# Kernel tuning notes

Measured on AMD Instinct MI355X. Metric: run time of the kernel, lower is better.

## Reference

```python
import jax, jax.numpy as jnp
import numpy as np
from jax import lax

EPS = 1e-5

# int4 fake-quant (Brevitas-style, per-tensor float scale)
# signed act: [-8, 7]; unsigned act: [0, 15]; weight narrow-range: [-7, 7]

def ste_round(x):
    # straight-through round (matches Brevitas STE; forward math == round)
    return x + lax.stop_gradient(jnp.round(x) - x)

def fq(x, s, lo, hi):
    return jnp.clip(ste_round(x / s), lo, hi) * s

def qw(w):
    # Int4WeightQuant: per-tensor scale from max-abs stats, narrow range [-7,7]
    s = jnp.max(jnp.abs(w)) / 7.0
    return jnp.clip(ste_round(w / s), -7.0, 7.0) * s

def conv(x, w, pad):
    return lax.conv_general_dilated(x, w, (1, 1), pad,
                                    dimension_numbers=('NCHW', 'OIHW', 'NCHW'))

def maxpool2(x):
    return lax.reduce_window(x, -jnp.inf, lax.max, (1, 1, 2, 2), (1, 1, 2, 2), 'VALID')

def bn_apply(x, bn):
    g, b, m, v = bn[0], bn[1], bn[2], bn[3]
    inv = g / jnp.sqrt(v + EPS)
    return x * inv[None, :, None, None] + (b - m * inv)[None, :, None, None]

def block(x, w, bn, s_in, s_relu, pool):
    x = fq(x, s_in, -8.0, 7.0)          # conv input_quant (signed int4)
    x = conv(x, qw(w), 'SAME')          # 3x3 quant conv, no bias
    x = bn_apply(x, bn)                 # BatchNorm (eval, running stats)
    x = jax.nn.relu(x)
    x = fq(x, s_relu, 0.0, 15.0)        # QuantReLU (unsigned int4)
    return maxpool2(x) if pool else x

def _forward(x, ws, b9, bns, scales):
    x = fq(x, scales[0], -8.0, 7.0)     # QuantIdentity (signed int4)
    for i in range(8):
        x = block(x, ws[i], bns[i], scales[1 + i], scales[10 + i], pool=(i < 4))
    x = fq(x, scales[9], -8.0, 7.0)     # head input_quant
    x = conv(x, qw(ws[8]), 'VALID') + b9[None, :, None, None]  # 1x1 head with bias
    return x


def setup_inputs() -> dict:
    key = jax.random.key(0)
    ks = jax.random.split(key, 32)
    B, H, W = 16, 320, 640
    x = jax.random.normal(ks[0], (B, 3, H, W), dtype=jnp.float32)
    wshapes = [(16, 3, 3, 3), (32, 16, 3, 3), (64, 32, 3, 3)] + [(64, 64, 3, 3)] * 5 + [(36, 64, 1, 1)]
    inp = {'x': x}
    for i, sh in enumerate(wshapes):
        inp[f'w{i+1}'] = 0.05 * jax.random.normal(ks[1 + i], sh, dtype=jnp.float32)
    inp['b9'] = 0.01 * jax.random.normal(ks[10], (36,), dtype=jnp.float32)
    chans = [16, 32, 64, 64, 64, 64, 64, 64]
    for i, c in enumerate(chans):
        k1, k2, k3, k4 = jax.random.split(ks[11 + i], 4)
        g = 0.75 + 0.5 * jax.random.uniform(k1, (c,), dtype=jnp.float32)
        b = 0.1 * jax.random.normal(k2, (c,), dtype=jnp.float32)
        m = 0.1 * jax.random.normal(k3, (c,), dtype=jnp.float32)
        v = 0.5 + 0.5 * jax.random.uniform(k4, (c,), dtype=jnp.float32)
        inp[f'bn{i+1}'] = jnp.stack([g, b, m, v])  # (4, C)
    inp['scales'] = 0.02 + 0.1 * jax.random.uniform(ks[30], (18,), dtype=jnp.float32)
    return inp


def reference(x, w1, w2, w3, w4, w5, w6, w7, w8, w9, b9,
              bn1, bn2, bn3, bn4, bn5, bn6, bn7, bn8, scales):
    ws = [w1, w2, w3, w4, w5, w6, w7, w8, w9]
    bns = [bn1, bn2, bn3, bn4, bn5, bn6, bn7, bn8]
    return _forward(x, ws, b9, bns, scales)
```

## Files before the change

### kernel.cpp

```cpp
#include <hip/hip_runtime.h>
#include <stdint.h>

#define EPSV 1e-5f

typedef int v4i __attribute__((ext_vector_type(4)));

__device__ __forceinline__ v4i mfma16(v4i a, v4i b, v4i c) {
    return __builtin_amdgcn_mfma_i32_16x16x64_i8(a, b, c, 0, 0, 0);
}

__device__ __forceinline__ int8_t q_epi(int s, float fscale, float inv, float beta,
                                        float s_relu, float s_next)
{
#pragma clang fp contract(off)
    float y = (float)s * fscale;
    y = y * inv;
    y = y + beta;
    float r = rintf(y / s_relu);
    r = fminf(fmaxf(r, 0.f), 15.f);
    float v = r * s_relu;
    float r2 = rintf(v / s_next);
    r2 = fminf(fmaxf(r2, -8.f), 7.f);
    return (int8_t)(int)r2;
}

struct WPtrs { const float* w[9]; int n[9]; };

__global__ __launch_bounds__(256) void k_wmax(WPtrs a, unsigned* __restrict__ smax)
{
    const int t = blockIdx.y;
    const int n = a.n[t];
    const float* w = a.w[t];
    float m = 0.f;
    for (int i = blockIdx.x * 256 + threadIdx.x; i < n; i += 16 * 256)
        m = fmaxf(m, fabsf(w[i]));
#pragma unroll
    for (int off = 32; off > 0; off >>= 1) m = fmaxf(m, __shfl_down(m, off));
    __shared__ float red[4];
    if ((threadIdx.x & 63) == 0) red[threadIdx.x >> 6] = m;
    __syncthreads();
    if (threadIdx.x == 0) {
        m = fmaxf(fmaxf(red[0], red[1]), fmaxf(red[2], red[3]));
        atomicMax(smax + t, __float_as_uint(m));
    }
}

struct PackArgs {
    const float* w[9];
    const float* bn[8];
    const unsigned* smax;
    int* qw;
    float* bnp;
};

#define NB_B    207
#define NB_HEAD 3
#define NB_BN   2

__global__ __launch_bounds__(256) void k_pack(PackArgs a)
{
#pragma clang fp contract(off)
    const int blk = blockIdx.x;
    if (blk < NB_B) {
        const int u = blk * 256 + threadIdx.x;
        const int bcum[9] = {0, 256, 1792, 6912, 16128, 25344, 34560, 43776, 52992};
        const int CIGA[8] = {1, 4, 8, 16, 16, 16, 16, 16};
        const int COA[8]  = {16, 32, 64, 64, 64, 64, 64, 64};
        const int NTA[8]  = {1, 2, 4, 4, 4, 4, 4, 4};
        const int CINA[8] = {3, 16, 32, 64, 64, 64, 64, 64};
        int L = 0;
        while (u >= bcum[L + 1]) ++L;
        const int rem = u - bcum[L];
        const int d = rem & 3;
        const int lane = (rem >> 2) & 63;
        const int gnt = rem >> 8;
        const int NT = NTA[L];
        const int nt = gnt % NT;
        const int g = gnt / NT;
        const int CIG = CIGA[L], CIN = CINA[L], CO = COA[L];
        const int TG = 16 / CIG;
        const int n = nt * 16 + (lane & 15);
        const float s = __uint_as_float(a.smax[L]) / 7.0f;
        const float* w = a.w[L];
        unsigned dw = 0;
        for (int jb = 0; jb < 4; ++jb) {
            const int k = 16 * (lane >> 4) + 4 * d + jb;
            const int tap = g * TG + k / (4 * CIG);
            const int ci = k % (4 * CIG);
            int qv = 0;
            if (tap < 9 && ci < CIN && n < CO) {
                float rr = rintf(w[(n * CIN + ci) * 9 + tap] / s);
                rr = fminf(fmaxf(rr, -7.f), 7.f);
                qv = (int)rr;
            }
            dw |= ((unsigned)(qv & 0xff)) << (8 * jb);
        }
        a.qw[u] = (int)dw;
    } else if (blk < NB_B + NB_HEAD) {
        const int uh = (blk - NB_B) * 256 + threadIdx.x;
        const int d = uh & 3;
        const int lane = (uh >> 2) & 63;
        const int nt = uh >> 8;
        const int n = nt * 16 + (lane & 15);
        const float s = __uint_as_float(a.smax[8]) / 7.0f;
        const float* w = a.w[8];
        unsigned dw = 0;
        for (int jb = 0; jb < 4; ++jb) {
            const int ci = 16 * (lane >> 4) + 4 * d + jb;
            int qv = 0;
            if (n < 36) {
                float rr = rintf(w[n * 64 + ci] / s);
                rr = fminf(fmaxf(rr, -7.f), 7.f);
                qv = (int)rr;
            }
            dw |= ((unsigned)(qv & 0xff)) << (8 * jb);
        }
        a.qw[52992 + uh] = (int)dw;
    } else {
        const int id = (blk - NB_B - NB_HEAD) * 256 + threadIdx.x;
        if (id >= 512) return;
        const int l = id >> 6, c = id & 63;
        const int C[8] = {16, 32, 64, 64, 64, 64, 64, 64};
        if (c < C[l]) {
            const float* bn = a.bn[l];
            const int Cl = C[l];
            float g = bn[c], b = bn[Cl + c], m = bn[2 * Cl + c], v = bn[3 * Cl + c];
            float inv = g / sqrtf(v + EPSV);
            float mi = m * inv;
            a.bnp[l * 128 + c] = inv;
            a.bnp[l * 128 + 64 + c] = b - mi;
        }
    }
}

__global__ __launch_bounds__(256) void k_conv0(
    const float* __restrict__ x, int8_t* __restrict__ out,
    const int* __restrict__ bfrag, const float* __restrict__ scales,
    const unsigned* __restrict__ smax, const float* __restrict__ bnp)
{
#pragma clang fp contract(off)
    __shared__ int tile[660];
    __shared__ float bnl[128];

    const int b = blockIdx.z;
    const int py0 = blockIdx.y * 4;
    const int px0 = blockIdx.x * 32;
    const int ty0 = 2 * py0 - 1;
    const int tx0 = 2 * px0 - 1;
    const float s0 = scales[0], s1 = scales[1];

    for (int i = threadIdx.x; i < 660; i += 256) {
        const int ly = i / 66;
        const int lx = i - ly * 66;
        const int gy = ty0 + ly, gx = tx0 + lx;
        int v = 0;
        if ((unsigned)gy < 320u && (unsigned)gx < 640u) {
#pragma unroll
            for (int ci = 0; ci < 3; ++ci) {
                float xv = x[((size_t)(b * 3 + ci) * 320 + gy) * 640 + gx];
                float r = rintf(xv / s0);
                r = fminf(fmaxf(r, -8.f), 7.f);
                float vv = r * s0;
                float r2 = rintf(vv / s1);
                r2 = fminf(fmaxf(r2, -8.f), 7.f);
                v |= ((int)r2 & 0xff) << (8 * ci);
            }
        }
        tile[i] = v;
    }
    if (threadIdx.x < 128) bnl[threadIdx.x] = bnp[threadIdx.x];

    const int lane = threadIdx.x & 63;
    const int wv = threadIdx.x >> 6;
    const v4i bfv = *(const v4i*)&bfrag[lane * 4];
    __syncthreads();

    const int q = lane >> 4;
    const int m = lane & 15;
    const int px_sub = m >> 2;
    const int op = m & 3;
    const int lyb = 2 * wv + (op >> 1);
    const int lxb0 = 2 * px_sub + (op & 1);

    const float sw = __uint_as_float(smax[0]) / 7.0f;
    const float fscale = scales[1] * sw;
    const float s_relu = scales[10];
    const float s_next = scales[2];
    const float inv = bnl[m];
    const float beta = bnl[64 + m];
    const int py = py0 + wv;

    for (int xs = 0; xs < 8; ++xs) {
        v4i af;
#pragma unroll
        for (int d = 0; d < 4; ++d) {
            int t = 4 * q + d; t = min(t, 8);
            const int ky = (t * 11) >> 5;
            const int kx = t - 3 * ky;
            af[d] = tile[(lyb + ky) * 66 + 8 * xs + lxb0 + kx];
        }
        v4i acc = mfma16(af, bfv, (v4i){0, 0, 0, 0});
        const int px = px0 + 4 * xs + q;
        const int s = max(max(acc[0], acc[1]), max(acc[2], acc[3]));
        out[((size_t)((b * 160 + py) * 320 + px)) * 16 + m] =
            q_epi(s, fscale, inv, beta, s_relu, s_next);
    }
}

template <int CIG, int CO, bool POOL, int H, int W, int XL, int NROWS, bool FUSED>
__global__ __launch_bounds__(256) void k_mconv(
    const int8_t* __restrict__ in, int8_t* __restrict__ out,
    const int* __restrict__ bfrag, const float* __restrict__ scales,
    const unsigned* __restrict__ smax, const float* __restrict__ bnp,
    int layer, int sin_idx, int srelu_idx, int snext_idx,
    const int* __restrict__ hfrag, const float* __restrict__ b9,
    float* __restrict__ dout)
{
    constexpr int NT = CO / 16;
    constexpr int TG = 16 / CIG;
    constexpr int NG = (9 + TG - 1) / TG;
    constexpr int WPR = POOL ? 1 : 2;
    constexpr int NTW = POOL ? NT : NT / 2;
    constexpr int OPW = POOL ? 4 : 16;
    constexpr int S = POOL ? 2 : 1;
    constexpr int TLH = S * NROWS + 2;
    constexpr int TLW = S * OPW * XL + 2;
    constexpr int TILE_DW = TLH * TLW * CIG;
    constexpr bool PRELOAD = (NG * NT <= 8);
    constexpr int Ho = POOL ? H / 2 : H;
    constexpr int Wo = POOL ? W / 2 : W;
    static_assert(WPR * NROWS == 4, "4 waves per block");
    static_assert(POOL || CIG == 16, "nonpool path assumes CIG=16");
    static_assert(!FUSED || (!POOL && XL == 1 && NROWS == 2), "fused head shape");

    __shared__ int tile[TILE_DW];
    __shared__ float bnl[128];
    __shared__ int code_dw[FUSED ? 512 : 1];

    const int b = blockIdx.z;
    const int py0 = blockIdx.y * NROWS;
    const int px0 = blockIdx.x * (OPW * XL);
    const int ty0 = S * py0 - 1;
    const int tx0 = S * px0 - 1;
    const int* gin = (const int*)in;

    for (int i = threadIdx.x; i < TILE_DW; i += 256) {
        const int cig = i & (CIG - 1);
        const int rest = i / CIG;
        const int lx = rest % TLW;
        const int ly = rest / TLW;
        const int gy = ty0 + ly, gx = tx0 + lx;
        int v = 0;
        if ((unsigned)gy < (unsigned)H && (unsigned)gx < (unsigned)W)
            v = gin[((b * H + gy) * W + gx) * CIG + cig];
        tile[i] = v;
    }
    if (threadIdx.x < 128) bnl[threadIdx.x] = bnp[layer * 128 + threadIdx.x];

    const int lane = threadIdx.x & 63;
    const int wv = threadIdx.x >> 6;
    v4i breg[PRELOAD ? NG * NT : 1];
    if constexpr (PRELOAD) {
#pragma unroll
        for (int i = 0; i < NG * NT; ++i)
            breg[i] = *(const v4i*)&bfrag[(i * 64 + lane) * 4];
    }
    __syncthreads();

    const int q = lane >> 4;
    const int m = lane & 15;

    const float swv = __uint_as_float(smax[layer]) / 7.0f;
    const float fscale = scales[sin_idx] * swv;
    const float s_relu = scales[srelu_idx];
    const float s_next = scales[snext_idx];

    int lyb, lxb0, wrow, nt0;
    if (POOL) {
        const int px_sub = m >> 2;
        const int op = m & 3;
        wrow = wv;
        nt0 = 0;
        lyb = 2 * wrow + (op >> 1);
        lxb0 = 2 * px_sub + (op & 1);
    } else {
        wrow = wv >> 1;
        nt0 = (wv & 1) * NTW;
        lyb = wrow;
        lxb0 = m;
    }

    for (int xs = 0; xs < XL; ++xs) {
        v4i acc[NTW];
#pragma unroll
        for (int j = 0; j < NTW; ++j) acc[j] = (v4i){0, 0, 0, 0};

#pragma unroll
        for (int g = 0; g < NG; ++g) {
            v4i af;
            if constexpr (CIG == 16) {
                const int ky = (g * 11) >> 5;
                const int kx = g - 3 * ky;
                int addr;
                if (POOL) addr = ((lyb + ky) * TLW + (8 * xs + lxb0 + kx)) * 16 + 4 * q;
                else      addr = ((lyb + ky) * TLW + (lxb0 + kx)) * 16 + 4 * q;
                af = *(const v4i*)&tile[addr];
            } else if constexpr (CIG == 8) {
                int t = 2 * g + (q >> 1); t = min(t, 8);
                const int ky = (t * 11) >> 5;
                const int kx = t - 3 * ky;
                const int addr = ((lyb + ky) * TLW + (8 * xs + lxb0 + kx)) * 8 + 4 * (q & 1);
                af = *(const v4i*)&tile[addr];
            } else if constexpr (CIG == 4) {
                int t = 4 * g + q; t = min(t, 8);
                const int ky = (t * 11) >> 5;
                const int kx = t - 3 * ky;
                const int addr = ((lyb + ky) * TLW + (8 * xs + lxb0 + kx)) * 4;
                af = *(const v4i*)&tile[addr];
            } else {
#pragma unroll
                for (int d = 0; d < 4; ++d) {
                    int t = 4 * q + d; t = min(t, 8);
                    const int ky = (t * 11) >> 5;
                    const int kx = t - 3 * ky;
                    af[d] = tile[(lyb + ky) * TLW + (8 * xs + lxb0 + kx)];
                }
            }
#pragma unroll
            for (int j = 0; j < NTW; ++j) {
                v4i bf;
                if constexpr (PRELOAD) bf = breg[g * NT + nt0 + j];
                else bf = *(const v4i*)&bfrag[((g * NT + nt0 + j) * 64 + lane) * 4];
                acc[j] = mfma16(af, bf, acc[j]);
            }
        }

        if (POOL) {
            const int py = py0 + wrow;
            const int px = px0 + 4 * xs + q;
            int8_t* po = out + ((size_t)((b * Ho + py) * Wo + px)) * CO + m;
#pragma unroll
            for (int j = 0; j < NTW; ++j) {
                const int co = j * 16 + m;
                const int s = max(max(acc[j][0], acc[j][1]), max(acc[j][2], acc[j][3]));
                po[j * 16] = q_epi(s, fscale, bnl[co], bnl[64 + co], s_relu, s_next);
            }
        } else {
            const int py = py0 + wrow;
#pragma unroll
            for (int j = 0; j < NTW; ++j) {
                const int co = (nt0 + j) * 16 + m;
                const float inv = bnl[co], beta = bnl[64 + co];
#pragma unroll
                for (int r = 0; r < 4; ++r) {
                    const int px = px0 + 4 * q + r;
                    const int8_t cb = q_epi(acc[j][r], fscale, inv, beta, s_relu, s_next);
                    if constexpr (FUSED) {
                        ((int8_t*)code_dw)[(wrow * 16 + 4 * q + r) * 64 + co] = cb;
                    } else {
                        if (px < Wo)
                            out[((size_t)((b * Ho + py) * Wo + px)) * CO + co] = cb;
                    }
                }
            }
        }
    }

    if constexpr (FUSED) {
        __syncthreads();
        if (wv < 2) {
#pragma clang fp contract(off)
            const v4i ha = *(const v4i*)&code_dw[(wv * 16 + m) * 16 + 4 * q];
            const float fs = scales[9] * (__uint_as_float(smax[8]) / 7.0f);
            const int py2 = py0 + wv;
#pragma unroll
            for (int nt = 0; nt < 3; ++nt) {
                const v4i hb = *(const v4i*)&hfrag[(nt * 64 + lane) * 4];
                const v4i hacc = mfma16(ha, hb, (v4i){0, 0, 0, 0});
                const int co = nt * 16 + m;
                if (co < 36) {
                    const float bias = b9[co];
#pragma unroll
                    for (int r = 0; r < 4; ++r) {
                        const int px = px0 + 4 * q + r;
                        if (px < 40) {
                            float y = (float)hacc[r] * fs;
                            dout[((size_t)(b * 36 + co)) * 800 + py2 * 40 + px] = y + bias;
                        }
                    }
                }
            }
        }
    }
}

extern "C" void kernel_launch(void* const* d_in, const int* in_sizes, int n_in,
                              void* d_out, int out_size, void* d_ws, size_t ws_size,
                              hipStream_t stream)
{
    const float* x = (const float*)d_in[0];
    const float* w[9];
    for (int i = 0; i < 9; i++) w[i] = (const float*)d_in[1 + i];
    const float* b9 = (const float*)d_in[10];
    const float* bn[8];
    for (int i = 0; i < 8; i++) bn[i] = (const float*)d_in[11 + i];
    const float* scales = (const float*)d_in[19];

    int8_t* base = (int8_t*)d_ws;
    int8_t* bufA = base;
    int8_t* bufB = base + 13107200;
    int*     qw  = (int*)(base + 26214400);
    unsigned* smax = (unsigned*)(base + 26429440);
    float*   bnp = (float*)(base + 26429952);

    static const int wn[9] = {432, 4608, 18432, 36864, 36864, 36864, 36864, 36864, 2304};
    static const int bo[8] = {0, 256, 1792, 6912, 16128, 25344, 34560, 43776};

    hipMemsetAsync(smax, 0, 9 * sizeof(unsigned), stream);

    WPtrs wp;
    for (int i = 0; i < 9; i++) { wp.w[i] = w[i]; wp.n[i] = wn[i]; }
    k_wmax<<<dim3(16, 9), 256, 0, stream>>>(wp, smax);

    PackArgs pa;
    for (int i = 0; i < 9; i++) pa.w[i] = w[i];
    for (int i = 0; i < 8; i++) pa.bn[i] = bn[i];
    pa.smax = smax; pa.qw = qw; pa.bnp = bnp;
    k_pack<<<NB_B + NB_HEAD + NB_BN, 256, 0, stream>>>(pa);

    k_conv0<<<dim3(10, 40, 16), 256, 0, stream>>>(
        x, bufB, qw + bo[0], scales, smax, bnp);

    k_mconv<4, 32, true, 160, 320, 4, 4, false><<<dim3(10, 20, 16), 256, 0, stream>>>(
        bufB, bufA, qw + bo[1], scales, smax, bnp, 1, 2, 11, 3, nullptr, nullptr, nullptr);
    k_mconv<8, 64, true, 80, 160, 2, 4, false><<<dim3(10, 10, 16), 256, 0, stream>>>(
        bufA, bufB, qw + bo[2], scales, smax, bnp, 2, 3, 12, 4, nullptr, nullptr, nullptr);
    k_mconv<16, 64, true, 40, 80, 1, 4, false><<<dim3(10, 5, 16), 256, 0, stream>>>(
        bufB, bufA, qw + bo[3], scales, smax, bnp, 3, 4, 13, 5, nullptr, nullptr, nullptr);
    k_mconv<16, 64, false, 20, 40, 1, 2, false><<<dim3(3, 10, 16), 256, 0, stream>>>(
        bufA, bufB, qw + bo[4], scales, smax, bnp, 4, 5, 14, 6, nullptr, nullptr, nullptr);
    k_mconv<16, 64, false, 20, 40, 1, 2, false><<<dim3(3, 10, 16), 256, 0, stream>>>(
        bufB, bufA, qw + bo[5], scales, smax, bnp, 5, 6, 15, 7, nullptr, nullptr, nullptr);
    k_mconv<16, 64, false, 20, 40, 1, 2, false><<<dim3(3, 10, 16), 256, 0, stream>>>(
        bufA, bufB, qw + bo[6], scales, smax, bnp, 6, 7, 16, 8, nullptr, nullptr, nullptr);
    k_mconv<16, 64, false, 20, 40, 1, 2, true><<<dim3(3, 10, 16), 256, 0, stream>>>(
        bufB, bufA, qw + bo[7], scales, smax, bnp, 7, 8, 17, 9,
        qw + 52992, b9, (float*)d_out);

    (void)in_sizes; (void)n_in; (void)out_size; (void)ws_size;
}
```

Before: 216.6 us.

## Fuse last four conv layers and head into one per-image LDS-resident kernel

Replaces the four non-pooled 20x40 conv launches and the fused head with a single k_tail kernel: one 1024-thread block per image keeps the whole activation map in LDS, ping-ponging between two buffers across layers. Activations are packed as int4 nibbles and sign-extended on the fly, which halves LDS footprint. This removes four kernel launches and the global round trips between layers. In exchange only 16 blocks run, so most CUs sit idle during the tail, and weight fragments are read from global memory inside the inner loop.

```diff
diff --git a/kernel.cpp b/kernel.cpp
--- a/kernel.cpp
+++ b/kernel.cpp
@@ -7,6 +7,15 @@
 
 __device__ __forceinline__ v4i mfma16(v4i a, v4i b, v4i c) {
     return __builtin_amdgcn_mfma_i32_16x16x64_i8(a, b, c, 0, 0, 0);
+}
+
+__device__ __forceinline__ int unlo(int p) {
+    int lo = p & 0x0F0F0F0F;
+    return lo | ((lo & 0x08080808) * 30);
+}
+__device__ __forceinline__ int unhi(int p) {
+    int hi = (p >> 4) & 0x0F0F0F0F;
+    return hi | ((hi & 0x08080808) * 30);
 }
 
 __device__ __forceinline__ int8_t q_epi(int s, float fscale, float inv, float beta,
@@ -182,8 +191,7 @@
     const int lyb = 2 * wv + (op >> 1);
     const int lxb0 = 2 * px_sub + (op & 1);
 
-    const float sw = __uint_as_float(smax[0]) / 7.0f;
-    const float fscale = scales[1] * sw;
+    const float fscale = scales[1] * (__uint_as_float(smax[0]) / 7.0f);
     const float s_relu = scales[10];
     const float s_next = scales[2];
     const float inv = bnl[m];
@@ -207,41 +215,31 @@
     }
 }
 
-template <int CIG, int CO, bool POOL, int H, int W, int XL, int NROWS, bool FUSED>
+template <int CIG, int CO, int H, int W, int XL>
 __global__ __launch_bounds__(256) void k_mconv(
     const int8_t* __restrict__ in, int8_t* __restrict__ out,
     const int* __restrict__ bfrag, const float* __restrict__ scales,
     const unsigned* __restrict__ smax, const float* __restrict__ bnp,
-    int layer, int sin_idx, int srelu_idx, int snext_idx,
-    const int* __restrict__ hfrag, const float* __restrict__ b9,
-    float* __restrict__ dout)
+    int layer, int sin_idx, int srelu_idx, int snext_idx)
 {
     constexpr int NT = CO / 16;
     constexpr int TG = 16 / CIG;
     constexpr int NG = (9 + TG - 1) / TG;
-    constexpr int WPR = POOL ? 1 : 2;
-    constexpr int NTW = POOL ? NT : NT / 2;
-    constexpr int OPW = POOL ? 4 : 16;
-    constexpr int S = POOL ? 2 : 1;
-    constexpr int TLH = S * NROWS + 2;
-    constexpr int TLW = S * OPW * XL + 2;
+    constexpr int TLH = 10;
+    constexpr int TLW = 8 * XL + 2;
     constexpr int TILE_DW = TLH * TLW * CIG;
     constexpr bool PRELOAD = (NG * NT <= 8);
-    constexpr int Ho = POOL ? H / 2 : H;
-    constexpr int Wo = POOL ? W / 2 : W;
-    static_assert(WPR * NROWS == 4, "4 waves per block");
-    static_assert(POOL || CIG == 16, "nonpool path assumes CIG=16");
-    static_assert(!FUSED || (!POOL && XL == 1 && NROWS == 2), "fused head shape");
+    constexpr int Ho = H / 2;
+    constexpr int Wo = W / 2;
 
     __shared__ int tile[TILE_DW];
     __shared__ float bnl[128];
-    __shared__ int code_dw[FUSED ? 512 : 1];
 
     const int b = blockIdx.z;
-    const int py0 = blockIdx.y * NROWS;
-    const int px0 = blockIdx.x * (OPW * XL);
-    const int ty0 = S * py0 - 1;
-    const int tx0 = S * px0 - 1;
+    const int py0 = blockIdx.y * 4;
+    const int px0 = blockIdx.x * (4 * XL);
+    const int ty0 = 2 * py0 - 1;
+    const int tx0 = 2 * px0 - 1;
     const int* gin = (const int*)in;
 
     for (int i = threadIdx.x; i < TILE_DW; i += 256) {
@@ -270,30 +268,19 @@
     const int q = lane >> 4;
     const int m = lane & 15;
 
-    const float swv = __uint_as_float(smax[layer]) / 7.0f;
-    const float fscale = scales[sin_idx] * swv;
+    const float fscale = scales[sin_idx] * (__uint_as_float(smax[layer]) / 7.0f);
     const float s_relu = scales[srelu_idx];
     const float s_next = scales[snext_idx];
 
-    int lyb, lxb0, wrow, nt0;
-    if (POOL) {
-        const int px_sub = m >> 2;
-        const int op = m & 3;
-        wrow = wv;
-        nt0 = 0;
-        lyb = 2 * wrow + (op >> 1);
-        lxb0 = 2 * px_sub + (op & 1);
-    } else {
-        wrow = wv >> 1;
-        nt0 = (wv & 1) * NTW;
-        lyb = wrow;
-        lxb0 = m;
-    }
+    const int px_sub = m >> 2;
+    const int op = m & 3;
+    const int lyb = 2 * wv + (op >> 1);
+    const int lxb0 = 2 * px_sub + (op & 1);
 
     for (int xs = 0; xs < XL; ++xs) {
-        v4i acc[NTW];
-#pragma unroll
-        for (int j = 0; j < NTW; ++j) acc[j] = (v4i){0, 0, 0, 0};
+        v4i acc[NT];
+#pragma unroll
+        for (int j = 0; j < NT; ++j) acc[j] = (v4i){0, 0, 0, 0};
 
 #pragma unroll
         for (int g = 0; g < NG; ++g) {
@@ -301,9 +288,7 @@
             if constexpr (CIG == 16) {
                 const int ky = (g * 11) >> 5;
                 const int kx = g - 3 * ky;
-                int addr;
-                if (POOL) addr = ((lyb + ky) * TLW + (8 * xs + lxb0 + kx)) * 16 + 4 * q;
-                else      addr = ((lyb + ky) * TLW + (lxb0 + kx)) * 16 + 4 * q;
+                const int addr = ((lyb + ky) * TLW + (8 * xs + lxb0 + kx)) * 16 + 4 * q;
                 af = *(const v4i*)&tile[addr];
             } else if constexpr (CIG == 8) {
                 int t = 2 * g + (q >> 1); t = min(t, 8);
@@ -317,77 +302,135 @@
                 const int kx = t - 3 * ky;
                 const int addr = ((lyb + ky) * TLW + (8 * xs + lxb0 + kx)) * 4;
                 af = *(const v4i*)&tile[addr];
-            } else {
-#pragma unroll
-                for (int d = 0; d < 4; ++d) {
-                    int t = 4 * q + d; t = min(t, 8);
-                    const int ky = (t * 11) >> 5;
-                    const int kx = t - 3 * ky;
-                    af[d] = tile[(lyb + ky) * TLW + (8 * xs + lxb0 + kx)];
-                }
-            }
-#pragma unroll
-            for (int j = 0; j < NTW; ++j) {
+            }
+#pragma unroll
+            for (int j = 0; j < NT; ++j) {
                 v4i bf;
-                if constexpr (PRELOAD) bf = breg[g * NT + nt0 + j];
-                else bf = *(const v4i*)&bfrag[((g * NT + nt0 + j) * 64 + lane) * 4];
+                if constexpr (PRELOAD) bf = breg[g * NT + j];
+                else bf = *(const v4i*)&bfrag[((g * NT + j) * 64 + lane) * 4];
                 acc[j] = mfma16(af, bf, acc[j]);
             }
         }
 
-        if (POOL) {
-            const int py = py0 + wrow;
-            const int px = px0 + 4 * xs + q;
-            int8_t* po = out + ((size_t)((b * Ho + py) * Wo + px)) * CO + m;
-#pragma unroll
-            for (int j = 0; j < NTW; ++j) {
-                const int co = j * 16 + m;
-                const int s = max(max(acc[j][0], acc[j][1]), max(acc[j][2], acc[j][3]));
-                po[j * 16] = q_epi(s, fscale, bnl[co], bnl[64 + co], s_relu, s_next);
-            }
-        } else {
-            const int py = py0 + wrow;
-#pragma unroll
-            for (int j = 0; j < NTW; ++j) {
-                const int co = (nt0 + j) * 16 + m;
-                const float inv = bnl[co], beta = bnl[64 + co];
+        const int py = py0 + wv;
+        const int px = px0 + 4 * xs + q;
+        int8_t* po = out + ((size_t)((b * Ho + py) * Wo + px)) * CO + m;
+#pragma unroll
+        for (int j = 0; j < NT; ++j) {
+            const int co = j * 16 + m;
+            const int s = max(max(acc[j][0], acc[j][1]), max(acc[j][2], acc[j][3]));
+            po[j * 16] = q_epi(s, fscale, bnl[co], bnl[64 + co], s_relu, s_next);
+        }
+    }
+}
+
+__global__ __launch_bounds__(1024) void k_tail(
+    const int8_t* __restrict__ in,
+    float* __restrict__ dout,
+    const int* __restrict__ qw,
+    const float* __restrict__ scales,
+    const unsigned* __restrict__ smax,
+    const float* __restrict__ bnp,
+    const float* __restrict__ b9)
+{
+    __shared__ int lbuf[2][7392];
+    __shared__ float bnl[512];
+
+    const int b = blockIdx.x;
+    const int tid = threadIdx.x;
+
+    for (int i = tid; i < 14784; i += 1024) ((int*)lbuf)[i] = 0;
+    for (int i = tid; i < 512; i += 1024) bnl[i] = bnp[512 + i];
+    __syncthreads();
+
+    const int* g = (const int*)in + (size_t)b * 12800;
+    for (int d = tid; d < 6400; d += 1024) {
+        const int px = d >> 3, dd = d & 7;
+        const int y = px / 40, x = px - y * 40;
+        const int dwA = g[px * 16 + dd];
+        const int dwB = g[px * 16 + dd + 8];
+        lbuf[0][((y + 1) * 42 + (x + 1)) * 8 + dd] =
+            (dwA & 0x0F0F0F0F) | ((dwB & 0x0F0F0F0F) << 4);
+    }
+    __syncthreads();
+
+    const int lane = tid & 63;
+    const int wv = tid >> 6;
+    const int q = lane >> 4;
+    const int m = lane & 15;
+    const int qoff = 4 * (q & 1);
+    const bool qlo = (q < 2);
+
+    const int bo4[4] = {16128, 25344, 34560, 43776};
+
+    for (int j = 0; j < 4; ++j) {
+        const int* src = lbuf[j & 1];
+        int* dst = lbuf[1 - (j & 1)];
+        const int* bf = qw + bo4[j];
+        const float fscale = scales[5 + j] * (__uint_as_float(smax[4 + j]) / 7.0f);
+        const float s_relu = scales[14 + j];
+        const float s_next = (j < 3) ? scales[6 + j] : scales[9];
+
+        for (int item = wv; item < 100; item += 16) {
+            const int t = item >> 1, ntl = item & 1;
+            const int p = t * 16 + m;
+            const int y = p / 40, x = p - y * 40;
+            v4i acc0 = (v4i){0, 0, 0, 0}, acc1 = (v4i){0, 0, 0, 0};
+#pragma unroll
+            for (int g9 = 0; g9 < 9; ++g9) {
+                const int ky = (g9 * 11) >> 5;
+                const int kx = g9 - 3 * ky;
+                const int base = ((y + ky) * 42 + (x + kx)) * 8 + qoff;
+                const int4 pk = *(const int4*)&src[base];
+                v4i af;
+                if (qlo) { af[0] = unlo(pk.x); af[1] = unlo(pk.y); af[2] = unlo(pk.z); af[3] = unlo(pk.w); }
+                else     { af[0] = unhi(pk.x); af[1] = unhi(pk.y); af[2] = unhi(pk.z); af[3] = unhi(pk.w); }
+                const v4i b0 = *(const v4i*)&bf[((g9 * 4 + ntl) * 64 + lane) * 4];
+                const v4i b1 = *(const v4i*)&bf[((g9 * 4 + ntl + 2) * 64 + lane) * 4];
+                acc0 = mfma16(af, b0, acc0);
+                acc1 = mfma16(af, b1, acc1);
+            }
+            const int co0 = ntl * 16 + m;
+            const int co1 = co0 + 32;
+            const float inv0 = bnl[j * 128 + co0], beta0 = bnl[j * 128 + 64 + co0];
+            const float inv1 = bnl[j * 128 + co1], beta1 = bnl[j * 128 + 64 + co1];
+#pragma unroll
+            for (int r = 0; r < 4; ++r) {
+                const int p2 = t * 16 + 4 * q + r;
+                const int y2 = p2 / 40, x2 = p2 - y2 * 40;
+                const int c0 = (int)q_epi(acc0[r], fscale, inv0, beta0, s_relu, s_next);
+                const int c1 = (int)q_epi(acc1[r], fscale, inv1, beta1, s_relu, s_next);
+                ((int8_t*)dst)[((y2 + 1) * 42 + (x2 + 1)) * 32 + m + 16 * ntl] =
+                    (int8_t)((c0 & 0xF) | ((c1 & 0xF) << 4));
+            }
+        }
+        __syncthreads();
+    }
+
+    {
+#pragma clang fp contract(off)
+        const int* src = lbuf[0];
+        const int* hf = qw + 52992;
+        const float fs = scales[9] * (__uint_as_float(smax[8]) / 7.0f);
+        for (int item = wv; item < 150; item += 16) {
+            const int t = item / 3, nt = item - 3 * t;
+            const int p = t * 16 + m;
+            const int y = p / 40, x = p - y * 40;
+            const int base = ((y + 1) * 42 + (x + 1)) * 8 + qoff;
+            const int4 pk = *(const int4*)&src[base];
+            v4i af;
+            if (qlo) { af[0] = unlo(pk.x); af[1] = unlo(pk.y); af[2] = unlo(pk.z); af[3] = unlo(pk.w); }
+            else     { af[0] = unhi(pk.x); af[1] = unhi(pk.y); af[2] = unhi(pk.z); af[3] = unhi(pk.w); }
+            const v4i bfv = *(const v4i*)&hf[(nt * 64 + lane) * 4];
+            const v4i acc = mfma16(af, bfv, (v4i){0, 0, 0, 0});
+            const int co = nt * 16 + m;
+            if (co < 36) {
+                const float bias = b9[co];
 #pragma unroll
                 for (int r = 0; r < 4; ++r) {
-                    const int px = px0 + 4 * q + r;
-                    const int8_t cb = q_epi(acc[j][r], fscale, inv, beta, s_relu, s_next);
-                    if constexpr (FUSED) {
-                        ((int8_t*)code_dw)[(wrow * 16 + 4 * q + r) * 64 + co] = cb;
-                    } else {
-                        if (px < Wo)
-                            out[((size_t)((b * Ho + py) * Wo + px)) * CO + co] = cb;
-                    }
-                }
-            }
-        }
-    }
-
-    if constexpr (FUSED) {
-        __syncthreads();
-        if (wv < 2) {
-#pragma clang fp contract(off)
-            const v4i ha = *(const v4i*)&code_dw[(wv * 16 + m) * 16 + 4 * q];
-            const float fs = scales[9] * (__uint_as_float(smax[8]) / 7.0f);
-            const int py2 = py0 + wv;
-#pragma unroll
-            for (int nt = 0; nt < 3; ++nt) {
-                const v4i hb = *(const v4i*)&hfrag[(nt * 64 + lane) * 4];
-                const v4i hacc = mfma16(ha, hb, (v4i){0, 0, 0, 0});
-                const int co = nt * 16 + m;
-                if (co < 36) {
-                    const float bias = b9[co];
-#pragma unroll
-                    for (int r = 0; r < 4; ++r) {
-                        const int px = px0 + 4 * q + r;
-                        if (px < 40) {
-                            float y = (float)hacc[r] * fs;
-                            dout[((size_t)(b * 36 + co)) * 800 + py2 * 40 + px] = y + bias;
-                        }
-                    }
+                    const int p2 = t * 16 + 4 * q + r;
+                    float yv = (float)acc[r] * fs;
+                    dout[((size_t)(b * 36 + co)) * 800 + p2] = yv + bias;
                 }
             }
         }
@@ -431,21 +474,15 @@
     k_conv0<<<dim3(10, 40, 16), 256, 0, stream>>>(
         x, bufB, qw + bo[0], scales, smax, bnp);
 
-    k_mconv<4, 32, true, 160, 320, 4, 4, false><<<dim3(10, 20, 16), 256, 0, stream>>>(
-        bufB, bufA, qw + bo[1], scales, smax, bnp, 1, 2, 11, 3, nullptr, nullptr, nullptr);
-    k_mconv<8, 64, true, 80, 160, 2, 4, false><<<dim3(10, 10, 16), 256, 0, stream>>>(
-        bufA, bufB, qw + bo[2], scales, smax, bnp, 2, 3, 12, 4, nullptr, nullptr, nullptr);
-    k_mconv<16, 64, true, 40, 80, 1, 4, false><<<dim3(10, 5, 16), 256, 0, stream>>>(
-        bufB, bufA, qw + bo[3], scales, smax, bnp, 3, 4, 13, 5, nullptr, nullptr, nullptr);
-    k_mconv<16, 64, false, 20, 40, 1, 2, false><<<dim3(3, 10, 16), 256, 0, stream>>>(
-        bufA, bufB, qw + bo[4], scales, smax, bnp, 4, 5, 14, 6, nullptr, nullptr, nullptr);
-    k_mconv<16, 64, false, 20, 40, 1, 2, false><<<dim3(3, 10, 16), 256, 0, stream>>>(
-        bufB, bufA, qw + bo[5], scales, smax, bnp, 5, 6, 15, 7, nullptr, nullptr, nullptr);
-    k_mconv<16, 64, false, 20, 40, 1, 2, false><<<dim3(3, 10, 16), 256, 0, stream>>>(
-        bufA, bufB, qw + bo[6], scales, smax, bnp, 6, 7, 16, 8, nullptr, nullptr, nullptr);
-    k_mconv<16, 64, false, 20, 40, 1, 2, true><<<dim3(3, 10, 16), 256, 0, stream>>>(
-        bufB, bufA, qw + bo[7], scales, smax, bnp, 7, 8, 17, 9,
-        qw + 52992, b9, (float*)d_out);
+    k_mconv<4, 32, 160, 320, 4><<<dim3(10, 20, 16), 256, 0, stream>>>(
+        bufB, bufA, qw + bo[1], scales, smax, bnp, 1, 2, 11, 3);
+    k_mconv<8, 64, 80, 160, 2><<<dim3(10, 10, 16), 256, 0, stream>>>(
+        bufA, bufB, qw + bo[2], scales, smax, bnp, 2, 3, 12, 4);
+    k_mconv<16, 64, 40, 80, 1><<<dim3(10, 5, 16), 256, 0, stream>>>(
+        bufB, bufA, qw + bo[3], scales, smax, bnp, 3, 4, 13, 5);
+
+    k_tail<<<16, 1024, 0, stream>>>(
+        bufA, (float*)d_out, qw, scales, smax, bnp, b9);
 
     (void)in_sizes; (void)n_in; (void)out_size; (void)ws_size;
 }
```

Result: slower. 294.2 us (+35.8%).
